# Optimization experiments

Measured on AMD Instinct MI355X. Metric: run time of the kernel, lower is better.

## Reference

```python
import jax, jax.numpy as jnp
import numpy as np

B, C, H, W_SP = 1024, 256, 8, 8
HID = 512


def setup_inputs() -> dict:
    key = jax.random.key(0)
    ks = jax.random.split(key, 7)
    s_in = 1.0 / np.sqrt(C)
    s_hid = 1.0 / np.sqrt(HID)
    return {
        "anchor": jax.random.normal(ks[0], (B, C, H, W_SP), dtype=jnp.float32),
        "positive": jax.random.normal(ks[1], (B, C, H, W_SP), dtype=jnp.float32),
        "W1": jax.random.uniform(ks[2], (HID, C), minval=-s_in, maxval=s_in, dtype=jnp.float32),
        "b1": jax.random.uniform(ks[3], (HID,), minval=-s_in, maxval=s_in, dtype=jnp.float32),
        "W2": jax.random.uniform(ks[4], (C, HID), minval=-s_hid, maxval=s_hid, dtype=jnp.float32),
        "b2": jax.random.uniform(ks[5], (C,), minval=-s_hid, maxval=s_hid, dtype=jnp.float32),
        "Ww": jax.random.uniform(ks[6], (C, C), minval=-s_in, maxval=s_in, dtype=jnp.float32),
    }


def reference(anchor, positive, W1, b1, W2, b2, Ww):
    b, c, h, w = anchor.shape
    # Flatten spatial dims: [h*w, b, c] (equivalent to iterating y then x)
    a = jnp.transpose(anchor, (2, 3, 0, 1)).reshape(h * w, b, c)
    p = jnp.transpose(positive, (2, 3, 0, 1)).reshape(h * w, b, c)
    # anchor_xy = anchor_xy + MLP(anchor_xy); MLP = Linear->ReLU->Linear
    hidden = jax.nn.relu(jnp.einsum('pbc,hc->pbh', a, W1) + b1)
    a = a + jnp.einsum('pbh,ch->pbc', hidden, W2) + b2
    # pred_xy = W(anchor_xy), no bias
    pred = jnp.einsum('pbc,dc->pbd', a, Ww)
    # logits[p] = pred[p] @ positive[p].T : [h*w, b, b]
    logits = jnp.einsum('pbd,pkd->pbk', pred, p)
    logits = logits - jnp.max(logits, axis=2, keepdims=True)
    return logits  # [h*w, b, b], stacked version of the original python list
```

## Files before the change

kernel.cpp:

```cpp
#include <hip/hip_runtime.h>

typedef unsigned short u16;
typedef short bf16x8 __attribute__((ext_vector_type(8)));
typedef float f32x4 __attribute__((ext_vector_type(4)));

__device__ inline u16 f2bf(float f) {
  unsigned u = __float_as_uint(f);
  u += 0x7fff + ((u >> 16) & 1);
  return (u16)(u >> 16);
}

__device__ inline void gl_lds16(const u16* g, u16* l) {
  __builtin_amdgcn_global_load_lds((const __attribute__((address_space(1))) void*)g,
                                   (__attribute__((address_space(3))) void*)l, 16, 0, 0);
}


__global__ __launch_bounds__(256) void cvt_bf16(const float* __restrict__ in,
                                                u16* __restrict__ outp, int n) {
  int i = blockIdx.x * 256 + threadIdx.x;
  if (i < n) outp[i] = f2bf(in[i]);
}

__global__ __launch_bounds__(256) void w2p_kernel(const float* __restrict__ Ww,
                                                  const float* __restrict__ W2,
                                                  const float* __restrict__ b2,
                                                  u16* __restrict__ W2p,
                                                  float* __restrict__ b2p) {
  int g = blockIdx.x * 256 + threadIdx.x;
  int d = g >> 9, h = g & 511;
  float s = 0.f;
  for (int c = 0; c < 256; c++) s += Ww[d * 256 + c] * W2[c * 512 + h];
  W2p[g] = f2bf(s);
  if (g < 256) {
    float t = 0.f;
    for (int c = 0; c < 256; c++) t += Ww[g * 256 + c] * b2[c];
    b2p[g] = t;
  }
}

__global__ __launch_bounds__(256) void transpose_cvt(const float* __restrict__ in,
                                                     u16* __restrict__ outp) {
  __shared__ u16 T[64 * 256];
  const int b = blockIdx.x;
  const int tid = threadIdx.x;
  const float4* in4 = (const float4*)in + (size_t)b * 4096;

  #pragma unroll
  for (int i = 0; i < 16; i++) {
    int local = i * 256 + tid;
    int c = local >> 4;
    int p4 = (local & 15) << 2;
    float4 v = in4[local];
    int cc = c >> 3, co = c & 7;
    #pragma unroll
    for (int k = 0; k < 4; k++) {
      int p = p4 + k;
      int chunk = p * 32 + (cc ^ ((p >> 2) & 15));
      float f = (k == 0) ? v.x : (k == 1) ? v.y : (k == 2) ? v.z : v.w;
      T[chunk * 8 + co] = f2bf(f);
    }
  }
  __syncthreads();

  u16* ob = outp + (size_t)b * 256;
  #pragma unroll
  for (int j = 0; j < 8; j++) {
    int idx = j * 256 + tid;
    int row = idx >> 5;
    int col16 = idx & 31;
    int chunk = row * 32 + (col16 ^ ((row >> 2) & 15));
    bf16x8 vv = *(const bf16x8*)&T[chunk * 8];
    *(bf16x8*)&ob[((size_t)row << 18) + col16 * 8] = vv;
  }
}

__global__ __launch_bounds__(256, 3)
void gemm_bt(const u16* __restrict__ A1, const u16* __restrict__ B1, int K1len,
             const u16* __restrict__ A2, const u16* __restrict__ B2, int K2len,
             const float* __restrict__ bias, u16* __restrict__ C, int N, int relu) {
  __shared__ u16 As[128 * 64];
  __shared__ u16 Bs[128 * 64];
  const int tid = threadIdx.x;
  const int lane = tid & 63;
  const int wave = tid >> 6;
  const int wm = wave & 1;
  const int wn = wave >> 1;
  const int m0 = blockIdx.y * 128;
  const int n0 = blockIdx.x * 128;
  const int q = lane >> 4;
  const int l15 = lane & 15;

  f32x4 acc[4][4];
  #pragma unroll
  for (int i = 0; i < 4; i++)
    #pragma unroll
    for (int j = 0; j < 4; j++) acc[i][j] = (f32x4)(0.0f);

  for (int seg = 0; seg < 2; seg++) {
    const u16* A = seg ? A2 : A1;
    const u16* B = seg ? B2 : B1;
    const int K = seg ? K2len : K1len;
    const int nkt = K >> 6;
    for (int kt = 0; kt < nkt; kt++) {
      #pragma unroll
      for (int c = 0; c < 4; c++) {
        int chunk = c * 256 + tid;
        int row = chunk >> 3;
        int cg = (chunk & 7) ^ (row & 7);
        gl_lds16(A + (size_t)(m0 + row) * K + kt * 64 + cg * 8, &As[chunk * 8]);
        gl_lds16(B + (size_t)(n0 + row) * K + kt * 64 + cg * 8, &Bs[chunk * 8]);
      }
      __syncthreads();
      #pragma unroll
      for (int ks = 0; ks < 2; ks++) {
        bf16x8 af[4], bfr[4];
        #pragma unroll
        for (int i = 0; i < 4; i++) {
          int row = wm * 64 + i * 16 + l15;
          af[i] = *(const bf16x8*)&As[row * 64 + (((ks * 4 + q) ^ (row & 7)) * 8)];
        }
        #pragma unroll
        for (int j = 0; j < 4; j++) {
          int row = wn * 64 + j * 16 + l15;
          bfr[j] = *(const bf16x8*)&Bs[row * 64 + (((ks * 4 + q) ^ (row & 7)) * 8)];
        }
        #pragma unroll
        for (int i = 0; i < 4; i++)
          #pragma unroll
          for (int j = 0; j < 4; j++)
            acc[i][j] = __builtin_amdgcn_mfma_f32_16x16x32_bf16(af[i], bfr[j], acc[i][j], 0, 0, 0);
      }
      __syncthreads();
    }
  }

  float bv[4];
  #pragma unroll
  for (int j = 0; j < 4; j++) bv[j] = bias[n0 + wn * 64 + j * 16 + l15];

  #pragma unroll
  for (int i = 0; i < 4; i++) {
    #pragma unroll
    for (int r = 0; r < 4; r++) {
      int row = m0 + wm * 64 + i * 16 + q * 4 + r;
      u16* crow = C + (size_t)row * N + n0 + wn * 64 + l15;
      #pragma unroll
      for (int j = 0; j < 4; j++) {
        float v = acc[i][j][r] + bv[j];
        if (relu) v = fmaxf(v, 0.0f);
        crow[j * 16] = f2bf(v);
      }
    }
  }
}

__global__ __launch_bounds__(512, 2)
void logits_k(const u16* __restrict__ pred, const u16* __restrict__ post,
              float* __restrict__ out) {
  __shared__ u16 As[64 * 256];
  __shared__ float pmax[8][64];
  const int tid = threadIdx.x;
  const int lane = tid & 63;
  const int wave = tid >> 6;
  const int q = lane >> 4;
  const int l15 = lane & 15;
  const int p = blockIdx.y;
  const int m0 = blockIdx.x * 64;
  const u16* Ap = pred + (((size_t)p * 1024 + m0) << 8);
  const u16* Bp = post + ((size_t)p << 18);

  #pragma unroll
  for (int c = 0; c < 4; c++) {
    int chunk = c * 512 + tid;
    int row = chunk >> 5;
    int cg = (chunk & 31) ^ (row & 7);
    gl_lds16(Ap + row * 256 + cg * 8, &As[chunk * 8]);
  }

  f32x4 acc[4][8];
  #pragma unroll
  for (int i = 0; i < 4; i++)
    #pragma unroll
    for (int j = 0; j < 8; j++) acc[i][j] = (f32x4)(0.0f);

  __syncthreads();

  const int nbase = wave * 128;
  #pragma unroll
  for (int kt = 0; kt < 8; kt++) {
    bf16x8 bfr[8];
    #pragma unroll
    for (int j = 0; j < 8; j++) {
      int n = nbase + j * 16 + l15;
      bfr[j] = *(const bf16x8*)&Bp[(size_t)n * 256 + kt * 32 + q * 8];
    }
    bf16x8 afr[4];
    #pragma unroll
    for (int i = 0; i < 4; i++) {
      int row = i * 16 + l15;
      afr[i] = *(const bf16x8*)&As[row * 256 + ((((kt << 2) + q) ^ (row & 7)) * 8)];
    }
    #pragma unroll
    for (int i = 0; i < 4; i++)
      #pragma unroll
      for (int j = 0; j < 8; j++)
        acc[i][j] = __builtin_amdgcn_mfma_f32_16x16x32_bf16(afr[i], bfr[j], acc[i][j], 0, 0, 0);
  }

  float rm[4][4];
  #pragma unroll
  for (int i = 0; i < 4; i++)
    #pragma unroll
    for (int r = 0; r < 4; r++) {
      float m = acc[i][0][r];
      #pragma unroll
      for (int j = 1; j < 8; j++) m = fmaxf(m, acc[i][j][r]);
      m = fmaxf(m, __shfl_xor(m, 1, 64));
      m = fmaxf(m, __shfl_xor(m, 2, 64));
      m = fmaxf(m, __shfl_xor(m, 4, 64));
      m = fmaxf(m, __shfl_xor(m, 8, 64));
      rm[i][r] = m;
    }
  if (l15 == 0) {
    #pragma unroll
    for (int i = 0; i < 4; i++)
      #pragma unroll
      for (int r = 0; r < 4; r++) pmax[wave][i * 16 + q * 4 + r] = rm[i][r];
  }
  __syncthreads();
  #pragma unroll
  for (int i = 0; i < 4; i++)
    #pragma unroll
    for (int r = 0; r < 4; r++) {
      int row = i * 16 + q * 4 + r;
      float m = pmax[0][row];
      #pragma unroll
      for (int w = 1; w < 8; w++) m = fmaxf(m, pmax[w][row]);
      rm[i][r] = m;
    }

  float* ob = out + ((size_t)p << 20) + (size_t)m0 * 1024 + nbase + l15;
  #pragma unroll
  for (int i = 0; i < 4; i++)
    #pragma unroll
    for (int r = 0; r < 4; r++) {
      float* orow = ob + (size_t)(i * 16 + q * 4 + r) * 1024;
      #pragma unroll
      for (int j = 0; j < 8; j++) orow[j * 16] = acc[i][j][r] - rm[i][r];
    }
}


extern "C" void kernel_launch(void* const* d_in, const int* in_sizes, int n_in,
                              void* d_out, int out_size, void* d_ws, size_t ws_size,
                              hipStream_t stream) {
  const float* anchor   = (const float*)d_in[0];
  const float* positive = (const float*)d_in[1];
  const float* W1       = (const float*)d_in[2];
  const float* b1       = (const float*)d_in[3];
  const float* W2       = (const float*)d_in[4];
  const float* b2       = (const float*)d_in[5];
  const float* Ww       = (const float*)d_in[6];
  float* out = (float*)d_out;
  char* ws = (char*)d_ws;

  u16*   A_t    = (u16*)(ws + 0x00000000);
  u16*   Pos_t  = (u16*)(ws + 0x02000000);
  u16*   hidden = (u16*)(ws + 0x04000000);
  u16*   pred   = (u16*)(ws + 0x08000000);
  u16*   W1b    = (u16*)(ws + 0x0A000000);
  u16*   Wwb    = (u16*)(ws + 0x0A100000);
  u16*   W2pb   = (u16*)(ws + 0x0A200000);
  float* b2p    = (float*)(ws + 0x0A300000);

  cvt_bf16<<<512, 256, 0, stream>>>(W1, W1b, 512 * 256);
  cvt_bf16<<<256, 256, 0, stream>>>(Ww, Wwb, 256 * 256);
  w2p_kernel<<<512, 256, 0, stream>>>(Ww, W2, b2, W2pb, b2p);
  transpose_cvt<<<1024, 256, 0, stream>>>(anchor, A_t);
  transpose_cvt<<<1024, 256, 0, stream>>>(positive, Pos_t);

  gemm_bt<<<dim3(4, 512), 256, 0, stream>>>(A_t, W1b, 256, nullptr, nullptr, 0,
                                            b1, hidden, 512, 1);
  gemm_bt<<<dim3(2, 512), 256, 0, stream>>>(A_t, Wwb, 256, hidden, W2pb, 512,
                                            b2p, pred, 256, 0);
  logits_k<<<dim3(16, 64), 512, 0, stream>>>(pred, Pos_t, out);
}
```

Baseline: 578.6 us.

## Fuse MLP hidden and prediction GEMMs into one kernel keeping hidden in LDS

Result: slower. 621.6 us (+7.4%).

```diff
diff --git a/kernel.cpp b/kernel.cpp
--- a/kernel.cpp
+++ b/kernel.cpp
@@ -75,83 +75,125 @@
   }
 }
 
-__global__ __launch_bounds__(256, 3)
-void gemm_bt(const u16* __restrict__ A1, const u16* __restrict__ B1, int K1len,
-             const u16* __restrict__ A2, const u16* __restrict__ B2, int K2len,
-             const float* __restrict__ bias, u16* __restrict__ C, int N, int relu) {
-  __shared__ u16 As[128 * 64];
-  __shared__ u16 Bs[128 * 64];
+
+#define GEMM_PHASE(ACC, BG, BSTRIDE, BCOL0, SRC)                                        \
+  _Pragma("unroll")                                                                      \
+  for (int kt = 0; kt < 8; kt++) {                                                       \
+    bf16x8 bfr[4];                                                                       \
+    _Pragma("unroll")                                                                    \
+    for (int j = 0; j < 4; j++) {                                                        \
+      int n = wn * 64 + j * 16 + l15;                                                    \
+      bfr[j] = *(const bf16x8*)&(BG)[(size_t)n * (BSTRIDE) + (BCOL0) + kt * 32 + q * 8]; \
+    }                                                                                    \
+    bf16x8 afr[4];                                                                       \
+    _Pragma("unroll")                                                                    \
+    for (int i = 0; i < 4; i++) {                                                        \
+      int row = wm * 64 + i * 16 + l15;                                                  \
+      afr[i] = *(const bf16x8*)&(SRC)[row * 256 + (((kt * 4 + q) ^ (row & 7)) * 8)];     \
+    }                                                                                    \
+    _Pragma("unroll")                                                                    \
+    for (int i = 0; i < 4; i++)                                                          \
+      _Pragma("unroll")                                                                  \
+      for (int j = 0; j < 4; j++)                                                        \
+        (ACC)[i][j] = __builtin_amdgcn_mfma_f32_16x16x32_bf16(afr[i], bfr[j], (ACC)[i][j], 0, 0, 0); \
+  }
+
+__global__ __launch_bounds__(512, 2)
+void mlp_pred(const u16* __restrict__ A, const u16* __restrict__ W1b,
+              const u16* __restrict__ W2pb, const u16* __restrict__ Wwb,
+              const float* __restrict__ b1, const float* __restrict__ b2p,
+              u16* __restrict__ pred) {
+  __shared__ u16 As[128 * 256];
+  __shared__ u16 Hs[128 * 256];
   const int tid = threadIdx.x;
   const int lane = tid & 63;
   const int wave = tid >> 6;
-  const int wm = wave & 1;
-  const int wn = wave >> 1;
-  const int m0 = blockIdx.y * 128;
-  const int n0 = blockIdx.x * 128;
+  const int wm = wave >> 2;
+  const int wn = wave & 3;
   const int q = lane >> 4;
   const int l15 = lane & 15;
-
-  f32x4 acc[4][4];
-  #pragma unroll
-  for (int i = 0; i < 4; i++)
-    #pragma unroll
-    for (int j = 0; j < 4; j++) acc[i][j] = (f32x4)(0.0f);
-
-  for (int seg = 0; seg < 2; seg++) {
-    const u16* A = seg ? A2 : A1;
-    const u16* B = seg ? B2 : B1;
-    const int K = seg ? K2len : K1len;
-    const int nkt = K >> 6;
-    for (int kt = 0; kt < nkt; kt++) {
-      #pragma unroll
-      for (int c = 0; c < 4; c++) {
-        int chunk = c * 256 + tid;
-        int row = chunk >> 3;
-        int cg = (chunk & 7) ^ (row & 7);
-        gl_lds16(A + (size_t)(m0 + row) * K + kt * 64 + cg * 8, &As[chunk * 8]);
-        gl_lds16(B + (size_t)(n0 + row) * K + kt * 64 + cg * 8, &Bs[chunk * 8]);
-      }
-      __syncthreads();
-      #pragma unroll
-      for (int ks = 0; ks < 2; ks++) {
-        bf16x8 af[4], bfr[4];
-        #pragma unroll
-        for (int i = 0; i < 4; i++) {
-          int row = wm * 64 + i * 16 + l15;
-          af[i] = *(const bf16x8*)&As[row * 64 + (((ks * 4 + q) ^ (row & 7)) * 8)];
-        }
+  const int m0 = blockIdx.x * 128;
+
+  #pragma unroll
+  for (int c = 0; c < 8; c++) {
+    int chunk = c * 512 + tid;
+    int row = chunk >> 5;
+    int cg = (chunk & 31) ^ (row & 7);
+    gl_lds16(A + (size_t)(m0 + row) * 256 + cg * 8, &As[chunk * 8]);
+  }
+
+  f32x4 acc_h[4][4], acc_p[4][4];
+  #pragma unroll
+  for (int i = 0; i < 4; i++)
+    #pragma unroll
+    for (int j = 0; j < 4; j++) { acc_h[i][j] = (f32x4)(0.0f); acc_p[i][j] = (f32x4)(0.0f); }
+
+  __syncthreads();
+
+  GEMM_PHASE(acc_h, W1b, 256, 0, As);
+  {
+    float bv[4];
+    #pragma unroll
+    for (int j = 0; j < 4; j++) bv[j] = b1[wn * 64 + j * 16 + l15];
+    #pragma unroll
+    for (int i = 0; i < 4; i++)
+      #pragma unroll
+      for (int r = 0; r < 4; r++) {
+        int row = wm * 64 + i * 16 + q * 4 + r;
         #pragma unroll
         for (int j = 0; j < 4; j++) {
-          int row = wn * 64 + j * 16 + l15;
-          bfr[j] = *(const bf16x8*)&Bs[row * 64 + (((ks * 4 + q) ^ (row & 7)) * 8)];
+          int col = wn * 64 + j * 16 + l15;
+          float v = fmaxf(acc_h[i][j][r] + bv[j], 0.0f);
+          Hs[row * 256 + (((col >> 3) ^ (row & 7)) << 3) + (col & 7)] = f2bf(v);
         }
+      }
+  }
+  __syncthreads();
+
+  GEMM_PHASE(acc_p, W2pb, 512, 0, Hs);
+  GEMM_PHASE(acc_p, Wwb, 256, 0, As);
+
+  #pragma unroll
+  for (int i = 0; i < 4; i++)
+    #pragma unroll
+    for (int j = 0; j < 4; j++) acc_h[i][j] = (f32x4)(0.0f);
+  GEMM_PHASE(acc_h, W1b + 256 * 256, 256, 0, As);
+
+  __syncthreads();
+  {
+    float bv[4];
+    #pragma unroll
+    for (int j = 0; j < 4; j++) bv[j] = b1[256 + wn * 64 + j * 16 + l15];
+    #pragma unroll
+    for (int i = 0; i < 4; i++)
+      #pragma unroll
+      for (int r = 0; r < 4; r++) {
+        int row = wm * 64 + i * 16 + q * 4 + r;
         #pragma unroll
-        for (int i = 0; i < 4; i++)
-          #pragma unroll
-          for (int j = 0; j < 4; j++)
-            acc[i][j] = __builtin_amdgcn_mfma_f32_16x16x32_bf16(af[i], bfr[j], acc[i][j], 0, 0, 0);
+        for (int j = 0; j < 4; j++) {
+          int col = wn * 64 + j * 16 + l15;
+          float v = fmaxf(acc_h[i][j][r] + bv[j], 0.0f);
+          Hs[row * 256 + (((col >> 3) ^ (row & 7)) << 3) + (col & 7)] = f2bf(v);
+        }
       }
-      __syncthreads();
-    }
-  }
-
-  float bv[4];
-  #pragma unroll
-  for (int j = 0; j < 4; j++) bv[j] = bias[n0 + wn * 64 + j * 16 + l15];
-
-  #pragma unroll
-  for (int i = 0; i < 4; i++) {
-    #pragma unroll
-    for (int r = 0; r < 4; r++) {
-      int row = m0 + wm * 64 + i * 16 + q * 4 + r;
-      u16* crow = C + (size_t)row * N + n0 + wn * 64 + l15;
-      #pragma unroll
-      for (int j = 0; j < 4; j++) {
-        float v = acc[i][j][r] + bv[j];
-        if (relu) v = fmaxf(v, 0.0f);
-        crow[j * 16] = f2bf(v);
+  }
+  __syncthreads();
+
+  GEMM_PHASE(acc_p, W2pb, 512, 256, Hs);
+
+  {
+    float bv[4];
+    #pragma unroll
+    for (int j = 0; j < 4; j++) bv[j] = b2p[wn * 64 + j * 16 + l15];
+    #pragma unroll
+    for (int i = 0; i < 4; i++)
+      #pragma unroll
+      for (int r = 0; r < 4; r++) {
+        int row = m0 + wm * 64 + i * 16 + q * 4 + r;
+        u16* crow = pred + (size_t)row * 256 + wn * 64 + l15;
+        #pragma unroll
+        for (int j = 0; j < 4; j++) crow[j * 16] = f2bf(acc_p[i][j][r] + bv[j]);
       }
-    }
   }
 }
 
@@ -267,7 +309,6 @@
 
   u16*   A_t    = (u16*)(ws + 0x00000000);
   u16*   Pos_t  = (u16*)(ws + 0x02000000);
-  u16*   hidden = (u16*)(ws + 0x04000000);
   u16*   pred   = (u16*)(ws + 0x08000000);
   u16*   W1b    = (u16*)(ws + 0x0A000000);
   u16*   Wwb    = (u16*)(ws + 0x0A100000);
@@ -280,9 +321,7 @@
   transpose_cvt<<<1024, 256, 0, stream>>>(anchor, A_t);
   transpose_cvt<<<1024, 256, 0, stream>>>(positive, Pos_t);
 
-  gemm_bt<<<dim3(4, 512), 256, 0, stream>>>(A_t, W1b, 256, nullptr, nullptr, 0,
-                                            b1, hidden, 512, 1);
-  gemm_bt<<<dim3(2, 512), 256, 0, stream>>>(A_t, Wwb, 256, hidden, W2pb, 512,
-                                            b2p, pred, 256, 0);
+  mlp_pred<<<512, 512, 0, stream>>>(A_t, W1b, W2pb, Wwb, b1, b2p, pred);
+
   logits_k<<<dim3(16, 64), 512, 0, stream>>>(pred, Pos_t, out);
 }
```

## Fuse MLP and prediction GEMMs into one kernel keeping hidden in LDS

Applied to the files above, without the earlier changes.

Measured after the change: 617.4 us. +6.7%, slower.

```diff
diff --git a/kernel.cpp b/kernel.cpp
--- a/kernel.cpp
+++ b/kernel.cpp
@@ -75,84 +75,122 @@
   }
 }
 
-__global__ __launch_bounds__(256, 3)
-void gemm_bt(const u16* __restrict__ A1, const u16* __restrict__ B1, int K1len,
-             const u16* __restrict__ A2, const u16* __restrict__ B2, int K2len,
-             const float* __restrict__ bias, u16* __restrict__ C, int N, int relu) {
-  __shared__ u16 As[128 * 64];
-  __shared__ u16 Bs[128 * 64];
+
+__global__ __launch_bounds__(256, 2)
+void mlp_pred(const u16* __restrict__ A, const u16* __restrict__ W1b,
+              const u16* __restrict__ W2pb, const u16* __restrict__ Wwb,
+              const float* __restrict__ b1, const float* __restrict__ b2p,
+              u16* __restrict__ pred) {
+  __shared__ u16 Hs[64 * 512];
   const int tid = threadIdx.x;
   const int lane = tid & 63;
   const int wave = tid >> 6;
-  const int wm = wave & 1;
-  const int wn = wave >> 1;
-  const int m0 = blockIdx.y * 128;
-  const int n0 = blockIdx.x * 128;
   const int q = lane >> 4;
   const int l15 = lane & 15;
-
-  f32x4 acc[4][4];
-  #pragma unroll
-  for (int i = 0; i < 4; i++)
-    #pragma unroll
-    for (int j = 0; j < 4; j++) acc[i][j] = (f32x4)(0.0f);
-
-  for (int seg = 0; seg < 2; seg++) {
-    const u16* A = seg ? A2 : A1;
-    const u16* B = seg ? B2 : B1;
-    const int K = seg ? K2len : K1len;
-    const int nkt = K >> 6;
-    for (int kt = 0; kt < nkt; kt++) {
-      #pragma unroll
-      for (int c = 0; c < 4; c++) {
-        int chunk = c * 256 + tid;
-        int row = chunk >> 3;
-        int cg = (chunk & 7) ^ (row & 7);
-        gl_lds16(A + (size_t)(m0 + row) * K + kt * 64 + cg * 8, &As[chunk * 8]);
-        gl_lds16(B + (size_t)(n0 + row) * K + kt * 64 + cg * 8, &Bs[chunk * 8]);
-      }
-      __syncthreads();
-      #pragma unroll
-      for (int ks = 0; ks < 2; ks++) {
-        bf16x8 af[4], bfr[4];
+  const int m0 = blockIdx.x * 64;
+  const u16* Ag = A + ((size_t)m0 << 8);
+
+  #pragma unroll
+  for (int half = 0; half < 2; half++) {
+    f32x4 acc[4][4];
+    #pragma unroll
+    for (int i = 0; i < 4; i++)
+      #pragma unroll
+      for (int j = 0; j < 4; j++) acc[i][j] = (f32x4)(0.0f);
+
+    const u16* Wh = W1b + ((size_t)(half * 256 + wave * 64) << 8);
+    #pragma unroll
+    for (int kt = 0; kt < 8; kt++) {
+      bf16x8 bfr[4];
+      #pragma unroll
+      for (int j = 0; j < 4; j++)
+        bfr[j] = *(const bf16x8*)&Wh[(size_t)(j * 16 + l15) * 256 + kt * 32 + q * 8];
+      bf16x8 afr[4];
+      #pragma unroll
+      for (int i = 0; i < 4; i++)
+        afr[i] = *(const bf16x8*)&Ag[(size_t)(i * 16 + l15) * 256 + kt * 32 + q * 8];
+      #pragma unroll
+      for (int i = 0; i < 4; i++)
         #pragma unroll
-        for (int i = 0; i < 4; i++) {
-          int row = wm * 64 + i * 16 + l15;
-          af[i] = *(const bf16x8*)&As[row * 64 + (((ks * 4 + q) ^ (row & 7)) * 8)];
-        }
+        for (int j = 0; j < 4; j++)
+          acc[i][j] = __builtin_amdgcn_mfma_f32_16x16x32_bf16(afr[i], bfr[j], acc[i][j], 0, 0, 0);
+    }
+
+    float bv[4];
+    #pragma unroll
+    for (int j = 0; j < 4; j++) bv[j] = b1[half * 256 + wave * 64 + j * 16 + l15];
+    #pragma unroll
+    for (int i = 0; i < 4; i++)
+      #pragma unroll
+      for (int r = 0; r < 4; r++) {
+        int row = i * 16 + q * 4 + r;
         #pragma unroll
         for (int j = 0; j < 4; j++) {
-          int row = wn * 64 + j * 16 + l15;
-          bfr[j] = *(const bf16x8*)&Bs[row * 64 + (((ks * 4 + q) ^ (row & 7)) * 8)];
+          int h = half * 256 + wave * 64 + j * 16 + l15;
+          float v = fmaxf(acc[i][j][r] + bv[j], 0.0f);
+          Hs[row * 512 + (((h >> 3) ^ (row & 7)) << 3) + (h & 7)] = f2bf(v);
         }
-        #pragma unroll
-        for (int i = 0; i < 4; i++)
-          #pragma unroll
-          for (int j = 0; j < 4; j++)
-            acc[i][j] = __builtin_amdgcn_mfma_f32_16x16x32_bf16(af[i], bfr[j], acc[i][j], 0, 0, 0);
       }
-      __syncthreads();
-    }
+  }
+
+  __syncthreads();
+
+  f32x4 acc[4][4];
+  #pragma unroll
+  for (int i = 0; i < 4; i++)
+    #pragma unroll
+    for (int j = 0; j < 4; j++) acc[i][j] = (f32x4)(0.0f);
+
+  const u16* Wd = Wwb + ((size_t)(wave * 64) << 8);
+  #pragma unroll
+  for (int kt = 0; kt < 8; kt++) {
+    bf16x8 bfr[4];
+    #pragma unroll
+    for (int j = 0; j < 4; j++)
+      bfr[j] = *(const bf16x8*)&Wd[(size_t)(j * 16 + l15) * 256 + kt * 32 + q * 8];
+    bf16x8 afr[4];
+    #pragma unroll
+    for (int i = 0; i < 4; i++)
+      afr[i] = *(const bf16x8*)&Ag[(size_t)(i * 16 + l15) * 256 + kt * 32 + q * 8];
+    #pragma unroll
+    for (int i = 0; i < 4; i++)
+      #pragma unroll
+      for (int j = 0; j < 4; j++)
+        acc[i][j] = __builtin_amdgcn_mfma_f32_16x16x32_bf16(afr[i], bfr[j], acc[i][j], 0, 0, 0);
+  }
+
+  const u16* W2w = W2pb + ((size_t)(wave * 64) << 9);
+  #pragma unroll
+  for (int kt = 0; kt < 16; kt++) {
+    bf16x8 bfr[4];
+    #pragma unroll
+    for (int j = 0; j < 4; j++)
+      bfr[j] = *(const bf16x8*)&W2w[(size_t)(j * 16 + l15) * 512 + kt * 32 + q * 8];
+    bf16x8 afr[4];
+    #pragma unroll
+    for (int i = 0; i < 4; i++) {
+      int row = i * 16 + l15;
+      afr[i] = *(const bf16x8*)&Hs[row * 512 + ((((kt << 2) + q) ^ (row & 7)) << 3)];
+    }
+    #pragma unroll
+    for (int i = 0; i < 4; i++)
+      #pragma unroll
+      for (int j = 0; j < 4; j++)
+        acc[i][j] = __builtin_amdgcn_mfma_f32_16x16x32_bf16(afr[i], bfr[j], acc[i][j], 0, 0, 0);
   }
 
   float bv[4];
   #pragma unroll
-  for (int j = 0; j < 4; j++) bv[j] = bias[n0 + wn * 64 + j * 16 + l15];
-
-  #pragma unroll
-  for (int i = 0; i < 4; i++) {
+  for (int j = 0; j < 4; j++) bv[j] = b2p[wave * 64 + j * 16 + l15];
+  #pragma unroll
+  for (int i = 0; i < 4; i++)
     #pragma unroll
     for (int r = 0; r < 4; r++) {
-      int row = m0 + wm * 64 + i * 16 + q * 4 + r;
-      u16* crow = C + (size_t)row * N + n0 + wn * 64 + l15;
-      #pragma unroll
-      for (int j = 0; j < 4; j++) {
-        float v = acc[i][j][r] + bv[j];
-        if (relu) v = fmaxf(v, 0.0f);
-        crow[j * 16] = f2bf(v);
-      }
-    }
-  }
+      int row = m0 + i * 16 + q * 4 + r;
+      u16* crow = pred + ((size_t)row << 8) + wave * 64 + l15;
+      #pragma unroll
+      for (int j = 0; j < 4; j++) crow[j * 16] = f2bf(acc[i][j][r] + bv[j]);
+    }
 }
 
 __global__ __launch_bounds__(512, 2)
@@ -267,7 +305,6 @@
 
   u16*   A_t    = (u16*)(ws + 0x00000000);
   u16*   Pos_t  = (u16*)(ws + 0x02000000);
-  u16*   hidden = (u16*)(ws + 0x04000000);
   u16*   pred   = (u16*)(ws + 0x08000000);
   u16*   W1b    = (u16*)(ws + 0x0A000000);
   u16*   Wwb    = (u16*)(ws + 0x0A100000);
@@ -280,9 +317,7 @@
   transpose_cvt<<<1024, 256, 0, stream>>>(anchor, A_t);
   transpose_cvt<<<1024, 256, 0, stream>>>(positive, Pos_t);
 
-  gemm_bt<<<dim3(4, 512), 256, 0, stream>>>(A_t, W1b, 256, nullptr, nullptr, 0,
-                                            b1, hidden, 512, 1);
-  gemm_bt<<<dim3(2, 512), 256, 0, stream>>>(A_t, Wwb, 256, hidden, W2pb, 512,
-                                            b2p, pred, 256, 0);
+  mlp_pred<<<1024, 256, 0, stream>>>(A_t, W1b, W2pb, Wwb, b1, b2p, pred);
+
   logits_k<<<dim3(16, 64), 512, 0, stream>>>(pred, Pos_t, out);
 }
```
